# Kernel optimization log

Measured on AMD Instinct MI355X. Metric: run time of the kernel, lower is better.

Reference implementation:

```python
import jax, jax.numpy as jnp
import numpy as np

B, L, D = 8, 4096, 512
KS = (3, 5, 7)
EPS = 1e-5
W_SCALE = 0.02  # tame torch.randn-style init for numerical sanity


def layernorm(x, g, b):
    mu = jnp.mean(x, axis=-1, keepdims=True)
    var = jnp.var(x, axis=-1, keepdims=True)
    return (x - mu) * jax.lax.rsqrt(var + EPS) * g + b


def masked_conv(x1, chain, W, b):
    # x1: (B, C, L); W: (O, C, K); chain: (B, L) int32
    K = W.shape[2]
    pad_l = (K - 1) // 2
    pad_r = (K - 1) - pad_l
    xp = jnp.pad(x1, ((0, 0), (0, 0), (pad_l, pad_r)))
    ip = jnp.pad(chain, ((0, 0), (pad_l, pad_r)))  # pad id = 0
    Lx = x1.shape[2]
    # center tap of each window is the position's own chain id (odd K, center == pad_l)
    out = b[None, :, None]
    for k in range(K):  # small static loop over taps
        xs = xp[:, :, k:k + Lx]                      # (B, C, L)
        mk = (ip[:, k:k + Lx] == chain)              # (B, L) bool
        out = out + jnp.einsum('bcl,oc->bol', xs * mk[:, None, :], W[:, :, k])
    return out


def setup_inputs() -> dict:
    key = jax.random.key(0)
    ks = jax.random.split(key, 16)
    inp = {
        'x': jax.random.normal(ks[0], (B, L, D), dtype=jnp.float32),
        'chain': jnp.sort(jax.random.randint(ks[1], (B, L), 0, 8), axis=-1).astype(jnp.int32),
    }
    for i, (name, K) in enumerate(zip(('W3', 'W5', 'W7'), KS)):
        inp[name] = jax.random.normal(ks[2 + i], (D, D, K), dtype=jnp.float32) * W_SCALE
        inp['b' + name[1:]] = jax.random.normal(ks[5 + i], (D,), dtype=jnp.float32) * W_SCALE
    inp['mlp_w1'] = jax.random.normal(ks[8], (D, 4 * D), dtype=jnp.float32) * W_SCALE
    inp['mlp_b1'] = jnp.zeros((4 * D,), dtype=jnp.float32)
    inp['mlp_w2'] = jax.random.normal(ks[9], (4 * D, D), dtype=jnp.float32) * W_SCALE
    inp['mlp_b2'] = jnp.zeros((D,), dtype=jnp.float32)
    inp['ln1_g'] = jnp.ones((D,), dtype=jnp.float32)
    inp['ln1_b'] = jnp.zeros((D,), dtype=jnp.float32)
    inp['ln2_g'] = jnp.ones((D,), dtype=jnp.float32)
    inp['ln2_b'] = jnp.zeros((D,), dtype=jnp.float32)
    return inp


def reference(x, chain, W3, b3, W5, b5, W7, b7,
              mlp_w1, mlp_b1, mlp_w2, mlp_b2,
              ln1_g, ln1_b, ln2_g, ln2_b):
    x1 = jnp.transpose(x, (0, 2, 1))  # (B, C, L)
    for W, b in ((W3, b3), (W5, b5), (W7, b7)):
        x1 = masked_conv(x1, chain, W, b)
    h = layernorm(x + jnp.transpose(x1, (0, 2, 1)), ln1_g, ln1_b)
    mlp = jax.nn.gelu(h @ mlp_w1 + mlp_b1) @ mlp_w2 + mlp_b2
    return layernorm(h + mlp, ln2_g, ln2_b)
```

## Files before the change

### kernel.cpp

```cpp
#include <hip/hip_runtime.h>
#include <math.h>

#define BB 8
#define LL 4096
#define DD 512
#define PTOT (BB*LL)
#define HID  2048

typedef __attribute__((ext_vector_type(8))) short short8;
typedef __attribute__((ext_vector_type(4))) float f32x4;

typedef __attribute__((address_space(1))) const unsigned int gconst_u32;
typedef __attribute__((address_space(3))) unsigned int lds_u32;

__device__ __forceinline__ void gload16(const void* g, void* l) {
    __builtin_amdgcn_global_load_lds((gconst_u32*)g, (lds_u32*)l, 16, 0, 0);
}

__device__ __forceinline__ unsigned short f2bf(float f) {
    union { float f; unsigned int u; } v; v.f = f;
    unsigned int r = v.u + 0x7fffu + ((v.u >> 16) & 1u);
    return (unsigned short)(r >> 16);
}
__device__ __forceinline__ float bf2f(unsigned short h) {
    union { unsigned int u; float f; } v; v.u = ((unsigned int)h) << 16;
    return v.f;
}
__device__ __forceinline__ float gelu_fast(float x) {
    float x2 = x * x;
    float t  = x * fmaf(0.044715f, x2, 1.0f);
    float e  = __builtin_amdgcn_exp2f(-2.3021143f * t);
    return x * __builtin_amdgcn_rcpf(1.0f + e);
}

__device__ __forceinline__ void barrier_sync() {
    asm volatile("" ::: "memory");
    __builtin_amdgcn_s_barrier();
    asm volatile("" ::: "memory");
}
#define WAITV(N) asm volatile("s_waitcnt vmcnt(" #N ")" ::: "memory")
#define WAITL0() asm volatile("s_waitcnt lgkmcnt(0)" ::: "memory")

__global__ __launch_bounds__(256) void convert_x(const float* __restrict__ x,
                                                 unsigned short* __restrict__ xb,
                                                 unsigned short* __restrict__ zp) {
    int tid = blockIdx.x * 256 + threadIdx.x;
    if (blockIdx.x == 0 && threadIdx.x < 128) zp[threadIdx.x] = 0;
    float4 v = ((const float4*)x)[tid];
    uint2 o;
    o.x = (unsigned int)f2bf(v.x) | ((unsigned int)f2bf(v.y) << 16);
    o.y = (unsigned int)f2bf(v.z) | ((unsigned int)f2bf(v.w) << 16);
    ((uint2*)xb)[tid] = o;
}

__global__ __launch_bounds__(256) void trans_wconv(const float* __restrict__ W,
                                                   unsigned short* __restrict__ Wt, int K) {
    int tid = blockIdx.x * 256 + threadIdx.x;
    if (tid >= DD * DD * K) return;
    int o  = tid / (K * DD);
    int kc = tid - o * K * DD;
    int k  = kc >> 9;
    int c  = kc & (DD - 1);
    Wt[tid] = f2bf(W[(o * DD + c) * K + k]);
}

__global__ __launch_bounds__(256) void trans_w1(const float* __restrict__ W,
                                                unsigned short* __restrict__ Wt) {
    int tid = blockIdx.x * 256 + threadIdx.x;
    int n = tid >> 9;
    int c = tid & (DD - 1);
    Wt[tid] = f2bf(W[c * HID + n]);
}

__global__ __launch_bounds__(256) void trans_w2(const float* __restrict__ W,
                                                unsigned short* __restrict__ Wt) {
    int tid = blockIdx.x * 256 + threadIdx.x;
    int n = tid >> 11;
    int h = tid & (HID - 1);
    Wt[tid] = f2bf(W[h * DD + n]);
}

__global__ __launch_bounds__(256) void make_srcp(const int* __restrict__ chain,
                                                 int* __restrict__ srcp, int K) {
    int tid = blockIdx.x * 256 + threadIdx.x;
    if (tid >= PTOT * K) return;
    int p = tid / K;
    int k = tid - p * K;
    int b = p >> 12;
    int l = p & (LL - 1);
    int pad = (K - 1) >> 1;
    int l2 = l + k - pad;
    bool ok = (l2 >= 0) && (l2 < LL) && (chain[b * LL + l2] == chain[b * LL + l]);
    srcp[tid] = ok ? (p + k - pad) : -1;
}

template <int TAPS, int EPI>
__global__ __launch_bounds__(512) void mfma_gemm2(
        const unsigned short* __restrict__ A, int lda,
        const int* __restrict__ srcp,
        const unsigned short* __restrict__ Bt, int ldb,
        const float* __restrict__ bias,
        void* __restrict__ Yv, int ldc, int Kspan,
        const unsigned short* __restrict__ zp) {
    __shared__ alignas(16) unsigned short As[2 * 256 * 64];
    __shared__ alignas(16) unsigned short Bs[2 * 256 * 64];
    __shared__ int srcp_s[TAPS > 0 ? 256 * TAPS : 4];

    const int t = threadIdx.x;
    const int lane = t & 63, w = t >> 6;
    const int wr = w & 1, wc = w >> 1;
    const int lm = lane & 15, qh = lane >> 4, x7 = lane & 7;
    const int qq = (lane & 7) ^ (lane >> 3);
    const int p0 = blockIdx.x * 256;
    const int o0 = blockIdx.y * 256;
    const int NKT = TAPS ? TAPS * 8 : (Kspan >> 6);

    f32x4 acc[8][4];
#pragma unroll
    for (int mi = 0; mi < 8; mi++)
#pragma unroll
        for (int nj = 0; nj < 4; nj++) acc[mi][nj] = (f32x4){0.f, 0.f, 0.f, 0.f};

    auto stg = [&](int h) {
        if (h >= 4 * NKT) return;
        int jt = h >> 2, ht = h & 3;
        unsigned short* dst = ((ht & 1) ? Bs : As)
                              + (jt & 1) * 16384 + ((ht >> 1) * 128 + w * 16) * 64;
        int kb = jt * 64;
#pragma unroll
        for (int i = 0; i < 2; i++) {
            int rl = (ht >> 1) * 128 + w * 16 + i * 8 + (lane >> 3);
            const unsigned short* g;
            if (ht & 1) {
                g = Bt + (size_t)(o0 + rl) * ldb + kb + qq * 8;
            } else if (TAPS) {
                int sp = srcp_s[rl * TAPS + (jt >> 3)];
                g = (sp >= 0) ? (A + (size_t)sp * lda + (jt & 7) * 64 + qq * 8) : zp;
            } else {
                g = A + (size_t)(p0 + rl) * lda + kb + qq * 8;
            }
            gload16(g, dst + i * 512);
        }
    };

    if (TAPS) {
        for (int idx = t; idx < 256 * TAPS; idx += 512)
            srcp_s[idx] = srcp[(size_t)p0 * TAPS + idx];
    }
    __syncthreads();
    stg(0); stg(1); stg(2); stg(3); stg(4); stg(5);
    WAITV(8);
    barrier_sync();

#define PH(BI, MIH, NJH, STG, TW) do {                                          \
    const unsigned short* as_ = As + (BI) * 16384;                              \
    const unsigned short* bs_ = Bs + (BI) * 16384;                              \
    short8 af[4][2], bf[2][2];                                                  \
    _Pragma("unroll")                                                           \
    for (int kk = 0; kk < 2; kk++) {                                            \
        int sa = ((kk * 4 + qh) ^ x7) * 8;                                      \
        _Pragma("unroll")                                                       \
        for (int m = 0; m < 4; m++)                                             \
            af[m][kk] = *(const short8*)&as_[((((MIH)*4+m)*2 + wr)*16 + lm)*64 + sa]; \
        _Pragma("unroll")                                                       \
        for (int n = 0; n < 2; n++)                                             \
            bf[n][kk] = *(const short8*)&bs_[((((NJH)*2+n)*4 + wc)*16 + lm)*64 + sa]; \
    }                                                                           \
    STG;                                                                        \
    barrier_sync();                                                             \
    WAITL0();                                                                   \
    __builtin_amdgcn_sched_barrier(0);                                          \
    __builtin_amdgcn_s_setprio(1);                                              \
    _Pragma("unroll")                                                           \
    for (int kk = 0; kk < 2; kk++)                                              \
        _Pragma("unroll")                                                       \
        for (int m = 0; m < 4; m++)                                             \
            _Pragma("unroll")                                                   \
            for (int n = 0; n < 2; n++)                                         \
                acc[(MIH)*4+m][(NJH)*2+n] = __builtin_amdgcn_mfma_f32_16x16x32_bf16( \
                    af[m][kk], bf[n][kk], acc[(MIH)*4+m][(NJH)*2+n], 0, 0, 0);  \
    __builtin_amdgcn_s_setprio(0);                                              \
    __builtin_amdgcn_sched_barrier(0);                                          \
    TW;                                                                         \
    barrier_sync();                                                             \
} while (0)

    for (int kt = 0; kt + 1 < NKT; ++kt) {
        int bi = kt & 1;
        PH(bi, 0, 0, stg(4 * kt + 6), WAITV(6));
        PH(bi, 0, 1, stg(4 * kt + 7), (void)0);
        PH(bi, 1, 0, stg(4 * kt + 8), (void)0);
        if (kt == NKT - 2) PH(bi, 1, 1, stg(4 * kt + 9), WAITV(4));
        else               PH(bi, 1, 1, stg(4 * kt + 9), WAITV(8));
    }
    {
        int bi = (NKT - 1) & 1;
        PH(bi, 0, 0, (void)0, WAITV(0));
        PH(bi, 0, 1, (void)0, (void)0);
        PH(bi, 1, 0, (void)0, (void)0);
        PH(bi, 1, 1, (void)0, (void)0);
    }
#undef PH

#pragma unroll
    for (int mi = 0; mi < 8; mi++) {
#pragma unroll
        for (int nj = 0; nj < 4; nj++) {
            int col = o0 + (nj * 4 + wc) * 16 + lm;
#pragma unroll
            for (int r = 0; r < 4; r++) {
                int row = p0 + (mi * 2 + wr) * 16 + qh * 4 + r;
                float v = acc[mi][nj][r];
                size_t idx = (size_t)row * ldc + col;
                if (EPI == 0) {
                    ((unsigned short*)Yv)[idx] = f2bf(v + bias[col]);
                } else if (EPI == 1) {
                    ((unsigned short*)Yv)[idx] = f2bf(gelu_fast(v + bias[col]));
                } else if (EPI == 2) {
                    ((float*)Yv)[idx] = v + bias[col];
                } else {
                    ((float*)Yv)[idx] += v;
                }
            }
        }
    }
}

__global__ __launch_bounds__(256) void ln1_kernel(const float* __restrict__ x,
                                                  const unsigned short* __restrict__ conv,
                                                  const float* __restrict__ g,
                                                  const float* __restrict__ beta,
                                                  unsigned short* __restrict__ h) {
    int p = blockIdx.x, t = threadIdx.x;
    size_t base = (size_t)p * DD;
    float v0 = x[base + t] + bf2f(conv[base + t]);
    float v1 = x[base + 256 + t] + bf2f(conv[base + 256 + t]);
    float s = v0 + v1, sq = v0 * v0 + v1 * v1;
#pragma unroll
    for (int off = 32; off > 0; off >>= 1) { s += __shfl_xor(s, off); sq += __shfl_xor(sq, off); }
    __shared__ float red[2][4];
    int wid = t >> 6, lane = t & 63;
    if (lane == 0) { red[0][wid] = s; red[1][wid] = sq; }
    __syncthreads();
    float S = red[0][0] + red[0][1] + red[0][2] + red[0][3];
    float SQ = red[1][0] + red[1][1] + red[1][2] + red[1][3];
    float mu = S * (1.f / DD);
    float var = SQ * (1.f / DD) - mu * mu;
    float rs = rsqrtf(var + 1e-5f);
    h[base + t]       = f2bf((v0 - mu) * rs * g[t] + beta[t]);
    h[base + 256 + t] = f2bf((v1 - mu) * rs * g[256 + t] + beta[256 + t]);
}

__global__ __launch_bounds__(256) void ln2_kernel(const unsigned short* __restrict__ h,
                                                  float* __restrict__ out,
                                                  const float* __restrict__ g,
                                                  const float* __restrict__ beta) {
    int p = blockIdx.x, t = threadIdx.x;
    size_t base = (size_t)p * DD;
    float v0 = bf2f(h[base + t]) + out[base + t];
    float v1 = bf2f(h[base + 256 + t]) + out[base + 256 + t];
    float s = v0 + v1, sq = v0 * v0 + v1 * v1;
#pragma unroll
    for (int off = 32; off > 0; off >>= 1) { s += __shfl_xor(s, off); sq += __shfl_xor(sq, off); }
    __shared__ float red[2][4];
    int wid = t >> 6, lane = t & 63;
    if (lane == 0) { red[0][wid] = s; red[1][wid] = sq; }
    __syncthreads();
    float S = red[0][0] + red[0][1] + red[0][2] + red[0][3];
    float SQ = red[1][0] + red[1][1] + red[1][2] + red[1][3];
    float mu = S * (1.f / DD);
    float var = SQ * (1.f / DD) - mu * mu;
    float rs = rsqrtf(var + 1e-5f);
    out[base + t]       = (v0 - mu) * rs * g[t] + beta[t];
    out[base + 256 + t] = (v1 - mu) * rs * g[256 + t] + beta[256 + t];
}

extern "C" void kernel_launch(void* const* d_in, const int* in_sizes, int n_in,
                              void* d_out, int out_size, void* d_ws, size_t ws_size,
                              hipStream_t stream) {
    const float* x     = (const float*)d_in[0];
    const int*   chain = (const int*)d_in[1];
    const float* W3    = (const float*)d_in[2];
    const float* b3    = (const float*)d_in[3];
    const float* W5    = (const float*)d_in[4];
    const float* b5    = (const float*)d_in[5];
    const float* W7    = (const float*)d_in[6];
    const float* b7    = (const float*)d_in[7];
    const float* w1    = (const float*)d_in[8];
    const float* bm1   = (const float*)d_in[9];
    const float* w2    = (const float*)d_in[10];
    const float* bm2   = (const float*)d_in[11];
    const float* g1    = (const float*)d_in[12];
    const float* be1   = (const float*)d_in[13];
    const float* g2    = (const float*)d_in[14];
    const float* be2   = (const float*)d_in[15];
    float* out = (float*)d_out;

    const size_t ACT = (size_t)PTOT * DD * 2;
    char* ws = (char*)d_ws;
    size_t off = 0;
    unsigned short* Xb   = (unsigned short*)(ws + off); off += ACT;
    unsigned short* buf1 = (unsigned short*)(ws + off); off += ACT;
    unsigned short* buf2 = (unsigned short*)(ws + off); off += ACT;
    unsigned short* w3t  = (unsigned short*)(ws + off); off += (size_t)3 * DD * DD * 2;
    unsigned short* w5t  = (unsigned short*)(ws + off); off += (size_t)5 * DD * DD * 2;
    unsigned short* w7t  = (unsigned short*)(ws + off); off += (size_t)7 * DD * DD * 2;
    unsigned short* w1t  = (unsigned short*)(ws + off); off += (size_t)DD * HID * 2;
    unsigned short* w2t  = (unsigned short*)(ws + off); off += (size_t)DD * HID * 2;
    int* srcp3 = (int*)(ws + off); off += (size_t)PTOT * 3 * 4;
    int* srcp5 = (int*)(ws + off); off += (size_t)PTOT * 5 * 4;
    int* srcp7 = (int*)(ws + off); off += (size_t)PTOT * 7 * 4;
    unsigned short* zp = (unsigned short*)(ws + off); off += 256;
    size_t base_off = off;
    bool full = (ws_size >= base_off + (size_t)PTOT * HID * 2);
    unsigned short* Hb = (unsigned short*)(ws + base_off);

    convert_x<<<PTOT * DD / (256 * 4), 256, 0, stream>>>(x, Xb, zp);
    trans_wconv<<<(DD * DD * 3 + 255) / 256, 256, 0, stream>>>(W3, w3t, 3);
    trans_wconv<<<(DD * DD * 5 + 255) / 256, 256, 0, stream>>>(W5, w5t, 5);
    trans_wconv<<<(DD * DD * 7 + 255) / 256, 256, 0, stream>>>(W7, w7t, 7);
    trans_w1<<<DD * HID / 256, 256, 0, stream>>>(w1, w1t);
    trans_w2<<<DD * HID / 256, 256, 0, stream>>>(w2, w2t);
    make_srcp<<<(PTOT * 3 + 255) / 256, 256, 0, stream>>>(chain, srcp3, 3);
    make_srcp<<<(PTOT * 5 + 255) / 256, 256, 0, stream>>>(chain, srcp5, 5);
    make_srcp<<<(PTOT * 7 + 255) / 256, 256, 0, stream>>>(chain, srcp7, 7);

    dim3 gconv(PTOT / 256, DD / 256);

    mfma_gemm2<3, 0><<<gconv, 512, 0, stream>>>(Xb, DD, srcp3, w3t, 3 * DD, b3, buf1, DD, DD, zp);
    mfma_gemm2<5, 0><<<gconv, 512, 0, stream>>>(buf1, DD, srcp5, w5t, 5 * DD, b5, buf2, DD, DD, zp);
    mfma_gemm2<7, 0><<<gconv, 512, 0, stream>>>(buf2, DD, srcp7, w7t, 7 * DD, b7, buf1, DD, DD, zp);

    ln1_kernel<<<PTOT, 256, 0, stream>>>(x, buf1, g1, be1, buf2);

    if (full) {
        dim3 g1d(PTOT / 256, HID / 256);
        mfma_gemm2<0, 1><<<g1d, 512, 0, stream>>>(buf2, DD, nullptr, w1t, DD, bm1,
                                                  Hb, HID, DD, zp);
        mfma_gemm2<0, 2><<<gconv, 512, 0, stream>>>(Hb, HID, nullptr, w2t, HID, bm2,
                                                    out, DD, HID, zp);
    } else {
        for (int jc = 0; jc < 4; jc++) {
            mfma_gemm2<0, 1><<<gconv, 512, 0, stream>>>(buf2, DD, nullptr,
                                                        w1t + (size_t)jc * DD * DD, DD,
                                                        bm1 + jc * DD, Hb, DD, DD, zp);
            if (jc == 0)
                mfma_gemm2<0, 2><<<gconv, 512, 0, stream>>>(Hb, DD, nullptr,
                                                            w2t + jc * DD, HID, bm2,
                                                            out, DD, DD, zp);
            else
                mfma_gemm2<0, 3><<<gconv, 512, 0, stream>>>(Hb, DD, nullptr,
                                                            w2t + jc * DD, HID, bm2,
                                                            out, DD, DD, zp);
        }
    }

    ln2_kernel<<<PTOT, 256, 0, stream>>>(buf2, out, g2, be2);
}
```

Before: 797.4 us.

## Restructure GEMM main loop to reuse B fragments and prefetch gather indices

The GEMM main loop is rewritten as a rolled loop (unroll 1) with separate A and B staging helpers. B fragments are read once per k-tile and reused across both M halves, and A fragments are reused across N halves, which cuts LDS reads. Gather indices for the masked-conv A operand are loaded from shared memory one phase ahead so the address lookup leaves the staging critical path. The wait counts change to match, and extra barriers per phase are added, which may cost synchronization overhead.

New measurement: 687.3 us. 13.8% less time.

```diff
diff --git a/kernel.cpp b/kernel.cpp
--- a/kernel.cpp
+++ b/kernel.cpp
@@ -40,6 +40,7 @@
 }
 #define WAITV(N) asm volatile("s_waitcnt vmcnt(" #N ")" ::: "memory")
 #define WAITL0() asm volatile("s_waitcnt lgkmcnt(0)" ::: "memory")
+#define SCHED0() __builtin_amdgcn_sched_barrier(0)
 
 __global__ __launch_bounds__(256) void convert_x(const float* __restrict__ x,
                                                  unsigned short* __restrict__ xb,
@@ -95,7 +96,7 @@
 }
 
 template <int TAPS, int EPI>
-__global__ __launch_bounds__(512) void mfma_gemm2(
+__global__ __launch_bounds__(512) void mfma_gemm3(
         const unsigned short* __restrict__ A, int lda,
         const int* __restrict__ srcp,
         const unsigned short* __restrict__ Bt, int ldb,
@@ -111,6 +112,7 @@
     const int wr = w & 1, wc = w >> 1;
     const int lm = lane & 15, qh = lane >> 4, x7 = lane & 7;
     const int qq = (lane & 7) ^ (lane >> 3);
+    const int l3 = lane >> 3;
     const int p0 = blockIdx.x * 256;
     const int o0 = blockIdx.y * 256;
     const int NKT = TAPS ? TAPS * 8 : (Kspan >> 6);
@@ -121,25 +123,43 @@
 #pragma unroll
         for (int nj = 0; nj < 4; nj++) acc[mi][nj] = (f32x4){0.f, 0.f, 0.f, 0.f};
 
-    auto stg = [&](int h) {
+    auto stgB = [&](int h) {
         if (h >= 4 * NKT) return;
-        int jt = h >> 2, ht = h & 3;
-        unsigned short* dst = ((ht & 1) ? Bs : As)
-                              + (jt & 1) * 16384 + ((ht >> 1) * 128 + w * 16) * 64;
-        int kb = jt * 64;
+        int jt = h >> 2;
+        int rb = (h & 2) ? 128 : 0;
+        unsigned short* dst = Bs + (jt & 1) * 16384 + (rb + w * 16) * 64;
+        int kb = jt << 6;
 #pragma unroll
         for (int i = 0; i < 2; i++) {
-            int rl = (ht >> 1) * 128 + w * 16 + i * 8 + (lane >> 3);
+            int rl = rb + w * 16 + i * 8 + l3;
+            gload16(Bt + (size_t)(o0 + rl) * ldb + kb + qq * 8, dst + i * 512);
+        }
+    };
+    auto stgA = [&](int h, int sp0, int sp1) {
+        if (h >= 4 * NKT) return;
+        int jt = h >> 2;
+        int rb = (h & 2) ? 128 : 0;
+        unsigned short* dst = As + (jt & 1) * 16384 + (rb + w * 16) * 64;
+#pragma unroll
+        for (int i = 0; i < 2; i++) {
             const unsigned short* g;
-            if (ht & 1) {
-                g = Bt + (size_t)(o0 + rl) * ldb + kb + qq * 8;
-            } else if (TAPS) {
-                int sp = srcp_s[rl * TAPS + (jt >> 3)];
+            if (TAPS) {
+                int sp = i ? sp1 : sp0;
                 g = (sp >= 0) ? (A + (size_t)sp * lda + (jt & 7) * 64 + qq * 8) : zp;
             } else {
-                g = A + (size_t)(p0 + rl) * lda + kb + qq * 8;
+                int rl = rb + w * 16 + i * 8 + l3;
+                g = A + (size_t)(p0 + rl) * lda + (jt << 6) + qq * 8;
             }
             gload16(g, dst + i * 512);
+        }
+    };
+    auto ldsp = [&](int h, int& sp0, int& sp1) {
+        if (TAPS && h < 4 * NKT) {
+            int jt = h >> 2, tap = jt >> 3;
+            int rb = (h & 2) ? 128 : 0;
+            int rl = rb + w * 16 + l3;
+            sp0 = srcp_s[rl * TAPS + tap];
+            sp1 = srcp_s[(rl + 8) * TAPS + tap];
         }
     };
 
@@ -148,28 +168,34 @@
             srcp_s[idx] = srcp[(size_t)p0 * TAPS + idx];
     }
     __syncthreads();
-    stg(0); stg(1); stg(2); stg(3); stg(4); stg(5);
-    WAITV(8);
+    int sp0 = -1, sp1 = -1;
+    ldsp(0, sp0, sp1); stgA(0, sp0, sp1);
+    stgB(1);
+    ldsp(2, sp0, sp1); stgA(2, sp0, sp1);
+    stgB(3);
+    ldsp(4, sp0, sp1); stgA(4, sp0, sp1);
+    stgB(5);
+    ldsp(6, sp0, sp1);
+    WAITV(4);
     barrier_sync();
 
-#define PH(BI, MIH, NJH, STG, TW) do {                                          \
-    const unsigned short* as_ = As + (BI) * 16384;                              \
-    const unsigned short* bs_ = Bs + (BI) * 16384;                              \
-    short8 af[4][2], bf[2][2];                                                  \
+#define RD_A(MIH) do {                                                          \
     _Pragma("unroll")                                                           \
     for (int kk = 0; kk < 2; kk++) {                                            \
         int sa = ((kk * 4 + qh) ^ x7) * 8;                                      \
         _Pragma("unroll")                                                       \
         for (int m = 0; m < 4; m++)                                             \
             af[m][kk] = *(const short8*)&as_[((((MIH)*4+m)*2 + wr)*16 + lm)*64 + sa]; \
+    } } while (0)
+#define RD_B(NJH, BF) do {                                                      \
+    _Pragma("unroll")                                                           \
+    for (int kk = 0; kk < 2; kk++) {                                            \
+        int sa = ((kk * 4 + qh) ^ x7) * 8;                                      \
         _Pragma("unroll")                                                       \
         for (int n = 0; n < 2; n++)                                             \
-            bf[n][kk] = *(const short8*)&bs_[((((NJH)*2+n)*4 + wc)*16 + lm)*64 + sa]; \
-    }                                                                           \
-    STG;                                                                        \
-    barrier_sync();                                                             \
-    WAITL0();                                                                   \
-    __builtin_amdgcn_sched_barrier(0);                                          \
+            BF[n][kk] = *(const short8*)&bs_[((((NJH)*2+n)*4 + wc)*16 + lm)*64 + sa]; \
+    } } while (0)
+#define MFMA_Q(MIH, NJH, BF)                                                    \
     __builtin_amdgcn_s_setprio(1);                                              \
     _Pragma("unroll")                                                           \
     for (int kk = 0; kk < 2; kk++)                                              \
@@ -178,29 +204,46 @@
             _Pragma("unroll")                                                   \
             for (int n = 0; n < 2; n++)                                         \
                 acc[(MIH)*4+m][(NJH)*2+n] = __builtin_amdgcn_mfma_f32_16x16x32_bf16( \
-                    af[m][kk], bf[n][kk], acc[(MIH)*4+m][(NJH)*2+n], 0, 0, 0);  \
+                    af[m][kk], BF[n][kk], acc[(MIH)*4+m][(NJH)*2+n], 0, 0, 0);  \
     __builtin_amdgcn_s_setprio(0);                                              \
-    __builtin_amdgcn_sched_barrier(0);                                          \
-    TW;                                                                         \
-    barrier_sync();                                                             \
-} while (0)
-
-    for (int kt = 0; kt + 1 < NKT; ++kt) {
-        int bi = kt & 1;
-        PH(bi, 0, 0, stg(4 * kt + 6), WAITV(6));
-        PH(bi, 0, 1, stg(4 * kt + 7), (void)0);
-        PH(bi, 1, 0, stg(4 * kt + 8), (void)0);
-        if (kt == NKT - 2) PH(bi, 1, 1, stg(4 * kt + 9), WAITV(4));
-        else               PH(bi, 1, 1, stg(4 * kt + 9), WAITV(8));
+    SCHED0()
+
+    short8 af[4][2], bf0[2][2], bf1[2][2];
+#pragma unroll 1
+    for (int kt = 0; kt < NKT; ++kt) {
+        const unsigned short* as_ = As + (kt & 1) * 16384;
+        const unsigned short* bs_ = Bs + (kt & 1) * 16384;
+        const bool last = (kt == NKT - 1);
+        RD_A(0); RD_B(0, bf0);
+        if (!last) stgA(4 * kt + 6, sp0, sp1);
+        barrier_sync();
+        WAITL0(); SCHED0();
+        MFMA_Q(0, 0, bf0);
+        if (!last) ldsp(4 * kt + 8, sp0, sp1);
+        barrier_sync();
+        RD_B(1, bf1);
+        if (!last) stgB(4 * kt + 7);
+        barrier_sync();
+        WAITL0(); SCHED0();
+        MFMA_Q(0, 1, bf1);
+        barrier_sync();
+        RD_A(1);
+        if (!last) stgA(4 * kt + 8, sp0, sp1);
+        barrier_sync();
+        WAITL0(); SCHED0();
+        MFMA_Q(1, 0, bf0);
+        if (!last) ldsp(4 * kt + 10, sp0, sp1);
+        barrier_sync();
+        if (!last) stgB(4 * kt + 9);
+        barrier_sync();
+        WAITL0(); SCHED0();
+        MFMA_Q(1, 1, bf1);
+        if (kt == NKT - 2) { WAITV(0); } else if (!last) { WAITV(4); }
+        barrier_sync();
     }
-    {
-        int bi = (NKT - 1) & 1;
-        PH(bi, 0, 0, (void)0, WAITV(0));
-        PH(bi, 0, 1, (void)0, (void)0);
-        PH(bi, 1, 0, (void)0, (void)0);
-        PH(bi, 1, 1, (void)0, (void)0);
-    }
-#undef PH
+#undef RD_A
+#undef RD_B
+#undef MFMA_Q
 
 #pragma unroll
     for (int mi = 0; mi < 8; mi++) {
@@ -327,29 +370,29 @@
 
     dim3 gconv(PTOT / 256, DD / 256);
 
-    mfma_gemm2<3, 0><<<gconv, 512, 0, stream>>>(Xb, DD, srcp3, w3t, 3 * DD, b3, buf1, DD, DD, zp);
-    mfma_gemm2<5, 0><<<gconv, 512, 0, stream>>>(buf1, DD, srcp5, w5t, 5 * DD, b5, buf2, DD, DD, zp);
-    mfma_gemm2<7, 0><<<gconv, 512, 0, stream>>>(buf2, DD, srcp7, w7t, 7 * DD, b7, buf1, DD, DD, zp);
+    mfma_gemm3<3, 0><<<gconv, 512, 0, stream>>>(Xb, DD, srcp3, w3t, 3 * DD, b3, buf1, DD, DD, zp);
+    mfma_gemm3<5, 0><<<gconv, 512, 0, stream>>>(buf1, DD, srcp5, w5t, 5 * DD, b5, buf2, DD, DD, zp);
+    mfma_gemm3<7, 0><<<gconv, 512, 0, stream>>>(buf2, DD, srcp7, w7t, 7 * DD, b7, buf1, DD, DD, zp);
 
     ln1_kernel<<<PTOT, 256, 0, stream>>>(x, buf1, g1, be1, buf2);
 
     if (full) {
         dim3 g1d(PTOT / 256, HID / 256);
-        mfma_gemm2<0, 1><<<g1d, 512, 0, stream>>>(buf2, DD, nullptr, w1t, DD, bm1,
+        mfma_gemm3<0, 1><<<g1d, 512, 0, stream>>>(buf2, DD, nullptr, w1t, DD, bm1,
                                                   Hb, HID, DD, zp);
-        mfma_gemm2<0, 2><<<gconv, 512, 0, stream>>>(Hb, HID, nullptr, w2t, HID, bm2,
+        mfma_gemm3<0, 2><<<gconv, 512, 0, stream>>>(Hb, HID, nullptr, w2t, HID, bm2,
                                                     out, DD, HID, zp);
     } else {
         for (int jc = 0; jc < 4; jc++) {
-            mfma_gemm2<0, 1><<<gconv, 512, 0, stream>>>(buf2, DD, nullptr,
+            mfma_gemm3<0, 1><<<gconv, 512, 0, stream>>>(buf2, DD, nullptr,
                                                         w1t + (size_t)jc * DD * DD, DD,
                                                         bm1 + jc * DD, Hb, DD, DD, zp);
             if (jc == 0)
-                mfma_gemm2<0, 2><<<gconv, 512, 0, stream>>>(Hb, DD, nullptr,
+                mfma_gemm3<0, 2><<<gconv, 512, 0, stream>>>(Hb, DD, nullptr,
                                                             w2t + jc * DD, HID, bm2,
                                                             out, DD, DD, zp);
             else
-                mfma_gemm2<0, 3><<<gconv, 512, 0, stream>>>(Hb, DD, nullptr,
+                mfma_gemm3<0, 3><<<gconv, 512, 0, stream>>>(Hb, DD, nullptr,
                                                             w2t + jc * DD, HID, bm2,
                                                             out, DD, DD, zp);
         }
```
